# Kernel optimization log

Measured on AMD Instinct MI355X. Metric: run time of the kernel, lower is better.

The kernel has to match this reference:

```python
import jax, jax.numpy as jnp
import numpy as np

EPS = 1e-5

def conv1d(x, w, b, pad):
    # x: (B,Cin,T), w: (Cout,Cin,K)
    y = jax.lax.conv_general_dilated(x, w, (1,), [(pad, pad)],
                                     dimension_numbers=('NCW', 'OIW', 'NCW'))
    return y + b[None, :, None]

def group_norm(x, scale, bias, groups):
    B, C, T = x.shape
    xg = x.reshape(B, groups, C // groups, T)
    mu = xg.mean(axis=(2, 3), keepdims=True)
    var = xg.var(axis=(2, 3), keepdims=True)
    xn = ((xg - mu) * jax.lax.rsqrt(var + EPS)).reshape(B, C, T)
    return xn * scale[None, :, None] + bias[None, :, None]

def setup_inputs() -> dict:
    key = jax.random.key(0)
    ks = jax.random.split(key, 16)
    T, B = 1024, 128
    class_size, style_size, char_style_size = 80, 256, 64
    hidden, n_out = 128, 1
    cin = class_size + style_size + char_style_size  # 400
    def w(k, shape, fan_in):
        return jax.random.normal(k, shape, jnp.float32) * (1.0 / np.sqrt(fan_in))
    inp = {
        'input': jax.random.normal(ks[0], (T, B, class_size), jnp.float32),
        'g_style': jax.random.normal(ks[1], (B, style_size), jnp.float32),
        'spacing_style': jax.random.normal(ks[2], (B, 8), jnp.float32),
        'char_style': jax.random.normal(ks[3], (B, class_size, char_style_size), jnp.float32),
        'conv1_w': w(ks[4], (hidden, cin, 3), cin * 3),
        'conv1_b': jnp.zeros((hidden,), jnp.float32),
        'gn1_s': jnp.ones((hidden,), jnp.float32),
        'gn1_b': jnp.zeros((hidden,), jnp.float32),
        'conv2_w': w(ks[5], (hidden // 2, hidden, 3), hidden * 3),
        'conv2_b': jnp.zeros((hidden // 2,), jnp.float32),
        'gn2_s': jnp.ones((hidden // 2,), jnp.float32),
        'gn2_b': jnp.zeros((hidden // 2,), jnp.float32),
        'conv3_w': w(ks[6], (hidden // 4, hidden // 2, 3), (hidden // 2) * 3),
        'conv3_b': jnp.zeros((hidden // 4,), jnp.float32),
        'gn3_s': jnp.ones((hidden // 4,), jnp.float32),
        'gn3_b': jnp.zeros((hidden // 4,), jnp.float32),
        'conv4_w': w(ks[7], (n_out, hidden // 4, 1), hidden // 4),
        'conv4_b': jnp.zeros((n_out,), jnp.float32),
        'mean': jnp.full((1, n_out), 2.0, jnp.float32),
        'std': jnp.full((1, n_out), 1.0, jnp.float32),
    }
    return inp

def reference(input, g_style, spacing_style, char_style,
              conv1_w, conv1_b, gn1_s, gn1_b,
              conv2_w, conv2_b, gn2_s, gn2_b,
              conv3_w, conv3_b, gn3_s, gn3_b,
              conv4_w, conv4_b, mean, std):
    T, B, _ = input.shape
    # vectorized char-style gather (replaces the python double loop)
    text_chars = jnp.argmax(input, axis=2)                      # (T,B)
    input_style = char_style[jnp.arange(B)[None, :], text_chars]  # (T,B,Dc)
    gs = jnp.broadcast_to(g_style[None], (T,) + g_style.shape)    # (T,B,Ds)
    x = jnp.concatenate([input, gs, input_style], axis=2)         # (T,B,Cin)
    x = x.transpose(1, 2, 0)                                      # (B,Cin,T)
    x = jax.nn.relu(group_norm(conv1d(x, conv1_w, conv1_b, 1), gn1_s, gn1_b, 32))
    x = jax.nn.relu(group_norm(conv1d(x, conv2_w, conv2_b, 1), gn2_s, gn2_b, 32))
    x = jax.nn.relu(group_norm(conv1d(x, conv3_w, conv3_b, 1), gn3_s, gn3_b, 32))
    x = conv1d(x, conv4_w, conv4_b, 0)                            # (B,n_out,T)
    out = x.transpose(2, 0, 1)                                    # (T,B,n_out)
    return out * std + mean
```

## Files before the change

### kernel.cpp

```cpp
#include <hip/hip_runtime.h>
#include <hip/hip_bf16.h>

#define T_LEN 1024
#define BATCH 128
#define NM 131072

typedef __attribute__((ext_vector_type(8))) short short8;
typedef __attribute__((ext_vector_type(4))) float f32x4;

__device__ __forceinline__ float b2f(ushort u) {
  union { uint i; float f; } c; c.i = ((uint)u) << 16; return c.f;
}
__device__ __forceinline__ ushort f2b(float f) {
  __hip_bfloat16 h = __float2bfloat16(f);
  return *reinterpret_cast<ushort*>(&h);
}
__device__ __forceinline__ uint pack2(float a, float b) {
  return (uint)f2b(a) | ((uint)f2b(b) << 16);
}

__global__ __launch_bounds__(256) void k_prep(const float* __restrict__ inp, const float* __restrict__ cs,
    const float* __restrict__ gsty,
    const float* __restrict__ w1, const float* __restrict__ b1,
    const float* __restrict__ w2, const float* __restrict__ w3,
    ushort* __restrict__ X1, float* __restrict__ Gfull, float* __restrict__ Gk0, float* __restrict__ Gk2,
    ushort* __restrict__ Wp1, ushort* __restrict__ Wp2, ushort* __restrict__ Wp3) {
  int bid = blockIdx.x, tid = threadIdx.x;
  if (bid < 1024) {
    __shared__ __align__(16) ushort L[4][32][160];
    int b0 = (bid >> 5) * 4;
    int t0 = (bid & 31) * 32;
    int q = tid & 3;
    int u = tid >> 2;
    int bp = u & 3;
    int tpA = u >> 2;
    int tpB = tpA + 16;
    int mA = (t0 + tpA)*128 + b0 + bp;
    int mB = (t0 + tpB)*128 + b0 + bp;
    const float* rpA = inp + (size_t)mA*80 + q*20;
    const float* rpB = inp + (size_t)mB*80 + q*20;
    float va[20], vb[20];
    #pragma unroll
    for (int i = 0; i < 5; ++i) {
      float4 ua = *(const float4*)(rpA + i*4);
      va[i*4+0]=ua.x; va[i*4+1]=ua.y; va[i*4+2]=ua.z; va[i*4+3]=ua.w;
    }
    #pragma unroll
    for (int i = 0; i < 5; ++i) {
      float4 ub = *(const float4*)(rpB + i*4);
      vb[i*4+0]=ub.x; vb[i*4+1]=ub.y; vb[i*4+2]=ub.z; vb[i*4+3]=ub.w;
    }
    {
      float best = va[0]; int bi = q*20;
      #pragma unroll
      for (int i = 1; i < 20; ++i) if (va[i] > best) { best = va[i]; bi = q*20 + i; }
      #pragma unroll
      for (int d = 1; d <= 2; d <<= 1) {
        float ob = __shfl_xor(best, d);
        int   oi = __shfl_xor(bi, d);
        if (ob > best || (ob == best && oi < bi)) { best = ob; bi = oi; }
      }
      ushort* lr = &L[bp][tpA][0];
      #pragma unroll
      for (int i = 0; i < 5; ++i) {
        uint2 pk; pk.x = pack2(va[i*4], va[i*4+1]); pk.y = pack2(va[i*4+2], va[i*4+3]);
        *(uint2*)(lr + q*20 + i*4) = pk;
      }
      *(uint2*)(lr + 80 + q*4) = make_uint2(0u, 0u);
      const float* crow = cs + ((size_t)(b0+bp)*80 + bi)*64 + q*16;
      #pragma unroll
      for (int i = 0; i < 4; ++i) {
        float4 uu = *(const float4*)(crow + i*4);
        uint2 pk; pk.x = pack2(uu.x, uu.y); pk.y = pack2(uu.z, uu.w);
        *(uint2*)(lr + 96 + q*16 + i*4) = pk;
      }
    }
    {
      float best = vb[0]; int bi = q*20;
      #pragma unroll
      for (int i = 1; i < 20; ++i) if (vb[i] > best) { best = vb[i]; bi = q*20 + i; }
      #pragma unroll
      for (int d = 1; d <= 2; d <<= 1) {
        float ob = __shfl_xor(best, d);
        int   oi = __shfl_xor(bi, d);
        if (ob > best || (ob == best && oi < bi)) { best = ob; bi = oi; }
      }
      ushort* lr = &L[bp][tpB][0];
      #pragma unroll
      for (int i = 0; i < 5; ++i) {
        uint2 pk; pk.x = pack2(vb[i*4], vb[i*4+1]); pk.y = pack2(vb[i*4+2], vb[i*4+3]);
        *(uint2*)(lr + q*20 + i*4) = pk;
      }
      *(uint2*)(lr + 80 + q*4) = make_uint2(0u, 0u);
      const float* crow = cs + ((size_t)(b0+bp)*80 + bi)*64 + q*16;
      #pragma unroll
      for (int i = 0; i < 4; ++i) {
        float4 uu = *(const float4*)(crow + i*4);
        uint2 pk; pk.x = pack2(uu.x, uu.y); pk.y = pack2(uu.z, uu.w);
        *(uint2*)(lr + 96 + q*16 + i*4) = pk;
      }
    }
    __syncthreads();
    int wave = tid >> 6, lane = tid & 63;
    ushort* dst = X1 + ((size_t)(b0 + wave)*1024 + t0)*160;
    const ushort* src = &L[wave][0][0];
    #pragma unroll
    for (int it = 0; it < 10; ++it) {
      int r = it*64 + lane;
      *(uint4*)(dst + r*8) = *(const uint4*)(src + r*8);
    }
  } else if (bid < 1152) {
    int b = bid - 1024;
    __shared__ float gl[256];
    gl[tid] = gsty[b*256 + tid];
    __syncthreads();
    if (tid < 128) {
      int o = tid;
      const float* wr = w1 + (size_t)o*1200 + 240;
      float s0 = 0.f, s1 = 0.f, s2 = 0.f;
      for (int c = 0; c < 256; ++c) {
        float g = gl[c];
        s0 += wr[c*3+0]*g; s1 += wr[c*3+1]*g; s2 += wr[c*3+2]*g;
      }
      Gk0[b*128+o] = s0;
      Gk2[b*128+o] = s2;
      Gfull[b*128+o] = s0 + s1 + s2 + b1[o];
    }
  } else {
    int e = (bid - 1152)*256 + tid;
    if (e < 61440) {
      int o = e / 480, r = e % 480, k = r / 160, c = r % 160;
      float v = 0.f;
      if (c < 80)       v = w1[(size_t)o*1200 + c*3 + k];
      else if (c >= 96) v = w1[(size_t)o*1200 + (336 + (c-96))*3 + k];
      Wp1[e] = f2b(v);
    } else if (e < 61440 + 24576) {
      int e2 = e - 61440;
      int o = e2/384, r = e2%384, k = r/128, c = r%128;
      Wp2[e2] = f2b(w2[(size_t)o*384 + c*3 + k]);
    } else if (e < 61440 + 24576 + 6144) {
      int e3 = e - 61440 - 24576;
      int o = e3/192, r = e3%192, k = r/64, c = r%64;
      Wp3[e3] = f2b(w3[(size_t)o*192 + c*3 + k]);
    }
  }
}

__device__ __forceinline__ uint4 c1_ldx(const ushort* X1b, int cc, int t0, int task) {
  int r = task >> 2, q = task & 3;
  int t = t0 - 1 + r;
  if (t >= 0 && t < T_LEN) return *(const uint4*)(X1b + (size_t)t*160 + cc*32 + q*8);
  return make_uint4(0u,0u,0u,0u);
}
__device__ __forceinline__ short8 c1_ldw(const ushort* Wp1, int cc, int task) {
  int o = task / 12, seg = task % 12;
  int k = seg >> 2, oct = seg & 3;
  return *(const short8*)(Wp1 + (size_t)o*480 + k*160 + cc*32 + oct*8);
}
__device__ __forceinline__ void c1_wrx(ushort (*Xsb)[40], int task, uint4 v) {
  int r = task >> 2, q = task & 3;
  *(uint4*)&Xsb[r][q*8] = v;
}
__device__ __forceinline__ void c1_wrw(ushort (*Wsb)[104], int task, short8 v) {
  int o = task / 12, seg = task % 12;
  *(short8*)&Wsb[o][seg*8] = v;
}

__global__ __launch_bounds__(256) void k_conv1(const ushort* __restrict__ X1, const ushort* __restrict__ Wp1,
    const float* __restrict__ Gfull, const float* __restrict__ Gk0, const float* __restrict__ Gk2,
    ushort* __restrict__ y1, float2* __restrict__ part1) {
  __shared__ __align__(16) ushort Xs[2][130][40];
  __shared__ __align__(16) ushort Ws[2][128][104];
  __shared__ float gf[128], g0v[128], g2v[128];
  __shared__ float ps[4][128], pq[4][128];
  int b = blockIdx.x, tt = blockIdx.y;
  int t0 = tt * 128;
  int tid = threadIdx.x, lane = tid & 63, wave = tid >> 6;
  int ln = lane & 15, lq = lane >> 4, wt = wave * 32;
  const ushort* X1b = X1 + (size_t)b * 163840;

  if (tid < 128) {
    gf[tid]  = Gfull[b*128 + tid];
    g0v[tid] = Gk0[b*128 + tid];
    g2v[tid] = Gk2[b*128 + tid];
  }
  f32x4 acc[2][8];
  #pragma unroll
  for (int m = 0; m < 2; ++m)
    #pragma unroll
    for (int n = 0; n < 8; ++n) { f32x4 z = {0.f,0.f,0.f,0.f}; acc[m][n] = z; }

  uint4 rx0, rx1, rx2;
  short8 rw[6];

  rx0 = c1_ldx(X1b, 0, t0, tid);
  rx1 = c1_ldx(X1b, 0, t0, tid + 256);
  if (tid < 8) rx2 = c1_ldx(X1b, 0, t0, tid + 512);
  #pragma unroll
  for (int i = 0; i < 6; ++i) rw[i] = c1_ldw(Wp1, 0, tid + i*256);
  c1_wrx(Xs[0], tid, rx0);
  c1_wrx(Xs[0], tid + 256, rx1);
  if (tid < 8) c1_wrx(Xs[0], tid + 512, rx2);
  #pragma unroll
  for (int i = 0; i < 6; ++i) c1_wrw(Ws[0], tid + i*256, rw[i]);
  __syncthreads();

  for (int cc = 0; cc < 5; ++cc) {
    bool more = (cc < 4);
    if (more) {
      rx0 = c1_ldx(X1b, cc+1, t0, tid);
      rx1 = c1_ldx(X1b, cc+1, t0, tid + 256);
      if (tid < 8) rx2 = c1_ldx(X1b, cc+1, t0, tid + 512);
      #pragma unroll
      for (int i = 0; i < 6; ++i) rw[i] = c1_ldw(Wp1, cc+1, tid + i*256);
    }
    int cur = cc & 1;
    #pragma unroll
    for (int k = 0; k < 3; ++k) {
      short8 a0 = *(const short8*)&Xs[cur][wt + ln + k][lq*8];
      short8 a1 = *(const short8*)&Xs[cur][wt + 16 + ln + k][lq*8];
      #pragma unroll
      for (int nt = 0; nt < 8; ++nt) {
        short8 bb = *(const short8*)&Ws[cur][nt*16 + ln][k*32 + lq*8];
        acc[0][nt] = __builtin_amdgcn_mfma_f32_16x16x32_bf16(a0, bb, acc[0][nt], 0, 0, 0);
        acc[1][nt] = __builtin_amdgcn_mfma_f32_16x16x32_bf16(a1, bb, acc[1][nt], 0, 0, 0);
      }
    }
    if (more) {
      int nxt = cur ^ 1;
      c1_wrx(Xs[nxt], tid, rx0);
      c1_wrx(Xs[nxt], tid + 256, rx1);
      if (tid < 8) c1_wrx(Xs[nxt], tid + 512, rx2);
      #pragma unroll
      for (int i = 0; i < 6; ++i) c1_wrw(Ws[nxt], tid + i*256, rw[i]);
    }
    __syncthreads();
  }

  #pragma unroll
  for (int nt = 0; nt < 8; ++nt) {
    int o = nt*16 + ln;
    float add = gf[o];
    float s = 0.f, sq = 0.f;
    #pragma unroll
    for (int mt = 0; mt < 2; ++mt) {
      int tb = t0 + wt + mt*16 + lq*4;
      float vv[4];
      #pragma unroll
      for (int r = 0; r < 4; ++r) {
        float v = acc[mt][nt][r] + add;
        int t = tb + r;
        if (t == 0) v -= g0v[o];
        if (t == T_LEN-1) v -= g2v[o];
        vv[r] = v; s += v; sq += v*v;
      }
      uint2 pk;
      pk.x = pack2(vv[0], vv[1]);
      pk.y = pack2(vv[2], vv[3]);
      *(uint2*)(y1 + ((size_t)b*128 + o)*T_LEN + tb) = pk;
    }
    s  += __shfl_xor(s, 16);  s  += __shfl_xor(s, 32);
    sq += __shfl_xor(sq, 16); sq += __shfl_xor(sq, 32);
    if (lane < 16) { ps[wave][o] = s; pq[wave][o] = sq; }
  }
  __syncthreads();
  if (tid < 128) {
    float S = ps[0][tid]+ps[1][tid]+ps[2][tid]+ps[3][tid];
    float Q = pq[0][tid]+pq[1][tid]+pq[2][tid]+pq[3][tid];
    part1[((size_t)b*128 + tid)*8 + tt] = make_float2(S, Q);
  }
}

__device__ __forceinline__ short8 mid_ldw(const ushort* Wp, int cin, int cc, int task) {
  int o = task / 12, seg = task % 12;
  int k = seg >> 2, oct = seg & 3;
  return *(const short8*)(Wp + ((size_t)o*3 + k)*cin + cc*32 + oct*8);
}
__device__ __forceinline__ void mid_wrw(ushort (*Wsb)[104], int task, short8 v) {
  int o = task / 12, seg = task % 12;
  *(short8*)&Wsb[o][seg*8] = v;
}

template<int NC, int CO, int NT, int CPG>
__global__ __launch_bounds__(256) void k_convmid(const ushort* __restrict__ xin,
    const ushort* __restrict__ Wp, const float* __restrict__ bias,
    const float2* __restrict__ partin, const float* __restrict__ gs, const float* __restrict__ gb,
    ushort* __restrict__ yout, float2* __restrict__ part) {
  constexpr int CIN = NC*32;
  constexpr int NG = CIN/CPG;
  __shared__ __align__(16) ushort Xs[2][130][40];
  __shared__ __align__(16) ushort Ws[2][CO][104];
  __shared__ float2 affl[CIN];
  __shared__ float ssb[CIN], qqb[CIN];
  __shared__ float2 gmr[NG];
  __shared__ float bl[CO];
  __shared__ float ps[4][CO], pq[4][CO];
  int b = blockIdx.x, tt = blockIdx.y, t0 = tt*128;
  int tid = threadIdx.x, lane = tid & 63, wave = tid >> 6;
  int ln = lane & 15, lq = lane >> 4, wt = wave*32;
  int cp = (tid & 15)*2, j = tid >> 4;
  int er = (tid < 32) ? 0 : 129, eci = tid & 31;
  const ushort* xb = xin + (size_t)b * CIN * T_LEN;

  if (tid < CIN) {
    const float2* p = partin + (size_t)(b*CIN + tid)*8;
    float S = 0.f, Q = 0.f;
    #pragma unroll
    for (int j2 = 0; j2 < 8; ++j2) { float2 v = p[j2]; S += v.x; Q += v.y; }
    ssb[tid] = S; qqb[tid] = Q;
  }
  if (tid < CO)  bl[tid]  = bias[tid];

  f32x4 acc[2][NT];
  #pragma unroll
  for (int m = 0; m < 2; ++m)
    #pragma unroll
    for (int n = 0; n < NT; ++n) { f32x4 z = {0.f,0.f,0.f,0.f}; acc[m][n] = z; }

  short8 v0, v1;
  ushort ev = 0;
  short8 rw0, rw1, rw2;
  int te = t0 - 1 + er;

  {
    const ushort* s0 = xb + (size_t)cp * T_LEN + t0 + j*8;
    v0 = *(const short8*)s0;
    v1 = *(const short8*)(s0 + T_LEN);
    ev = 0;
    if (tid < 64 && te >= 0 && te < T_LEN) ev = xb[(size_t)eci * T_LEN + te];
    rw0 = mid_ldw(Wp, CIN, 0, tid);
    if constexpr (CO == 64) {
      rw1 = mid_ldw(Wp, CIN, 0, tid + 256);
      rw2 = mid_ldw(Wp, CIN, 0, tid + 512);
    } else {
      if (tid < 128) rw1 = mid_ldw(Wp, CIN, 0, tid + 256);
    }
  }
  __syncthreads();
  if (tid < NG) {
    float S = 0.f, Q = 0.f;
    #pragma unroll
    for (int ci = 0; ci < CPG; ++ci) { S += ssb[tid*CPG+ci]; Q += qqb[tid*CPG+ci]; }
    float invn = 1.f / (float)(CPG * T_LEN);
    float m = S * invn;
    float var = Q * invn - m*m;
    gmr[tid] = make_float2(m, rsqrtf(var + 1e-5f));
  }
  __syncthreads();
  if (tid < CIN) {
    float2 mr = gmr[tid / CPG];
    float a = mr.y * gs[tid];
    affl[tid] = make_float2(a, gb[tid] - mr.x * a);
  }
  __syncthreads();
  {
    float2 A0 = affl[cp], A1 = affl[cp+1];
    #pragma unroll
    for (int e = 0; e < 8; ++e) {
      float f0 = fmaxf(0.f, b2f((ushort)v0[e])*A0.x + A0.y);
      float f1 = fmaxf(0.f, b2f((ushort)v1[e])*A1.x + A1.y);
      *(uint*)&Xs[0][1 + j*8 + e][cp] = pack2(f0, f1);
    }
    if (tid < 64) {
      ushort val = 0;
      if (te >= 0 && te < T_LEN) { float2 A = affl[eci]; val = f2b(fmaxf(0.f, b2f(ev)*A.x + A.y)); }
      Xs[0][er][eci] = val;
    }
    mid_wrw(Ws[0], tid, rw0);
    if constexpr (CO == 64) {
      mid_wrw(Ws[0], tid + 256, rw1);
      mid_wrw(Ws[0], tid + 512, rw2);
    } else {
      if (tid < 128) mid_wrw(Ws[0], tid + 256, rw1);
    }
  }
  __syncthreads();

  for (int cc = 0; cc < NC; ++cc) {
    bool more = (cc + 1 < NC);
    if (more) {
      const ushort* s0 = xb + (size_t)((cc+1)*32 + cp) * T_LEN + t0 + j*8;
      v0 = *(const short8*)s0;
      v1 = *(const short8*)(s0 + T_LEN);
      ev = 0;
      if (tid < 64 && te >= 0 && te < T_LEN) ev = xb[(size_t)((cc+1)*32 + eci) * T_LEN + te];
      rw0 = mid_ldw(Wp, CIN, cc+1, tid);
      if constexpr (CO == 64) {
        rw1 = mid_ldw(Wp, CIN, cc+1, tid + 256);
        rw2 = mid_ldw(Wp, CIN, cc+1, tid + 512);
      } else {
        if (tid < 128) rw1 = mid_ldw(Wp, CIN, cc+1, tid + 256);
      }
    }
    int cur = cc & 1;
    #pragma unroll
    for (int k = 0; k < 3; ++k) {
      short8 a0 = *(const short8*)&Xs[cur][wt + ln + k][lq*8];
      short8 a1 = *(const short8*)&Xs[cur][wt + 16 + ln + k][lq*8];
      #pragma unroll
      for (int nt = 0; nt < NT; ++nt) {
        short8 bb = *(const short8*)&Ws[cur][nt*16 + ln][k*32 + lq*8];
        acc[0][nt] = __builtin_amdgcn_mfma_f32_16x16x32_bf16(a0, bb, acc[0][nt], 0, 0, 0);
        acc[1][nt] = __builtin_amdgcn_mfma_f32_16x16x32_bf16(a1, bb, acc[1][nt], 0, 0, 0);
      }
    }
    if (more) {
      int nxt = cur ^ 1;
      float2 A0 = affl[(cc+1)*32 + cp], A1 = affl[(cc+1)*32 + cp + 1];
      #pragma unroll
      for (int e = 0; e < 8; ++e) {
        float f0 = fmaxf(0.f, b2f((ushort)v0[e])*A0.x + A0.y);
        float f1 = fmaxf(0.f, b2f((ushort)v1[e])*A1.x + A1.y);
        *(uint*)&Xs[nxt][1 + j*8 + e][cp] = pack2(f0, f1);
      }
      if (tid < 64) {
        ushort val = 0;
        if (te >= 0 && te < T_LEN) { float2 A = affl[(cc+1)*32 + eci]; val = f2b(fmaxf(0.f, b2f(ev)*A.x + A.y)); }
        Xs[nxt][er][eci] = val;
      }
      mid_wrw(Ws[nxt], tid, rw0);
      if constexpr (CO == 64) {
        mid_wrw(Ws[nxt], tid + 256, rw1);
        mid_wrw(Ws[nxt], tid + 512, rw2);
      } else {
        if (tid < 128) mid_wrw(Ws[nxt], tid + 256, rw1);
      }
    }
    __syncthreads();
  }

  #pragma unroll
  for (int nt = 0; nt < NT; ++nt) {
    int o = nt*16 + ln;
    float add = bl[o];
    float s = 0.f, sq = 0.f;
    #pragma unroll
    for (int mt = 0; mt < 2; ++mt) {
      int tb = t0 + wt + mt*16 + lq*4;
      float vv[4];
      #pragma unroll
      for (int r = 0; r < 4; ++r) {
        float v = acc[mt][nt][r] + add;
        vv[r] = v; s += v; sq += v*v;
      }
      uint2 pk;
      pk.x = pack2(vv[0], vv[1]);
      pk.y = pack2(vv[2], vv[3]);
      *(uint2*)(yout + ((size_t)b*CO + o)*T_LEN + tb) = pk;
    }
    s  += __shfl_xor(s, 16);  s  += __shfl_xor(s, 32);
    sq += __shfl_xor(sq, 16); sq += __shfl_xor(sq, 32);
    if (lane < 16) { ps[wave][o] = s; pq[wave][o] = sq; }
  }
  __syncthreads();
  if (tid < CO) {
    float S = ps[0][tid]+ps[1][tid]+ps[2][tid]+ps[3][tid];
    float Q = pq[0][tid]+pq[1][tid]+pq[2][tid]+pq[3][tid];
    part[((size_t)b*CO + tid)*8 + tt] = make_float2(S, Q);
  }
}

__global__ __launch_bounds__(256) void k_final(const ushort* __restrict__ y3, const float2* __restrict__ part3,
    const float* __restrict__ s3, const float* __restrict__ b3,
    const float* __restrict__ w4, const float* __restrict__ b4,
    const float* __restrict__ mn, const float* __restrict__ sd, float* __restrict__ out) {
  int b = blockIdx.x;
  int t = blockIdx.y * 256 + threadIdx.x;
  __shared__ float wl[32];
  __shared__ float2 al[32];
  if (threadIdx.x < 32) {
    int c = threadIdx.x;
    const float2* p = part3 + (size_t)(b*32 + c)*8;
    float S = 0.f, Q = 0.f;
    #pragma unroll
    for (int j = 0; j < 8; ++j) { float2 v = p[j]; S += v.x; Q += v.y; }
    float invn = 1.f / (float)T_LEN;
    float m = S * invn;
    float var = Q * invn - m*m;
    float rs = rsqrtf(var + 1e-5f);
    float a = rs * s3[c];
    al[c] = make_float2(a, b3[c] - m*a);
    wl[c] = w4[c];
  }
  __syncthreads();
  float s = b4[0];
  #pragma unroll 8
  for (int c = 0; c < 32; ++c) {
    float v = b2f(y3[((size_t)b*32 + c)*T_LEN + t]);
    float2 A = al[c];
    s += wl[c] * fmaxf(0.f, v*A.x + A.y);
  }
  out[(size_t)t*BATCH + b] = s*sd[0] + mn[0];
}

extern "C" void kernel_launch(void* const* d_in, const int* in_sizes, int n_in,
                              void* d_out, int out_size, void* d_ws, size_t ws_size,
                              hipStream_t stream) {
  const float* inp  = (const float*)d_in[0];
  const float* gsty = (const float*)d_in[1];
  const float* cs   = (const float*)d_in[3];
  const float* w1   = (const float*)d_in[4];
  const float* b1   = (const float*)d_in[5];
  const float* gn1s = (const float*)d_in[6];
  const float* gn1b = (const float*)d_in[7];
  const float* w2   = (const float*)d_in[8];
  const float* b2   = (const float*)d_in[9];
  const float* gn2s = (const float*)d_in[10];
  const float* gn2b = (const float*)d_in[11];
  const float* w3   = (const float*)d_in[12];
  const float* b3   = (const float*)d_in[13];
  const float* gn3s = (const float*)d_in[14];
  const float* gn3b = (const float*)d_in[15];
  const float* w4   = (const float*)d_in[16];
  const float* b4   = (const float*)d_in[17];
  const float* mn   = (const float*)d_in[18];
  const float* sd   = (const float*)d_in[19];
  float* out = (float*)d_out;
  ushort* wsu = (ushort*)d_ws;

  ushort* X1  = wsu;
  ushort* Wp1 = X1 + (size_t)20971520;
  ushort* Wp2 = Wp1 + 61440;
  ushort* Wp3 = Wp2 + 24576;
  float* Gfull = (float*)(Wp3 + 6144);
  float* Gk0   = Gfull + 16384;
  float* Gk2   = Gk0 + 16384;
  ushort* y1 = (ushort*)(Gk2 + 16384);
  ushort* y2 = y1 + (size_t)NM*128;
  ushort* y3 = y2 + (size_t)NM*64;
  float2* part1 = (float2*)(y3 + (size_t)NM*32);
  float2* part2 = part1 + 131072;
  float2* part3 = part2 + 65536;

  k_prep<<<1512, 256, 0, stream>>>(inp, cs, gsty, w1, b1, w2, w3,
                                   X1, Gfull, Gk0, Gk2, Wp1, Wp2, Wp3);
  k_conv1<<<dim3(128,8), 256, 0, stream>>>(X1, Wp1, Gfull, Gk0, Gk2, y1, part1);
  k_convmid<4,64,4,4><<<dim3(128,8), 256, 0, stream>>>(y1, Wp2, b2, part1, gn1s, gn1b, y2, part2);
  k_convmid<2,32,2,2><<<dim3(128,8), 256, 0, stream>>>(y2, Wp3, b3, part2, gn2s, gn2b, y3, part3);
  k_final<<<dim3(128,4), 256, 0, stream>>>(y3, part3, gn3s, gn3b, w4, b4, mn, sd, out);
}
```

Measured before the change: 95.95 us.

## Read one-hot input directly in conv1 and shrink intermediate buffer to char-style only

The prep kernel no longer writes the 80 input channels plus padding into a 160-wide bf16 staging tensor. It now stores only the 64 gathered char-style channels. conv1 reads and converts the fp32 input channels straight from the original tensor for the first three channel chunks, and reads the compact char-style buffer for the last two. This cuts the staging buffer's write and read traffic. In exchange, conv1 loads fp32 data with strided per-timestep access (stride B*80) and does the bf16 conversion itself.

New measurement: 95.56 us. About the same (-0.4%).

```diff
diff --git a/kernel.cpp b/kernel.cpp
--- a/kernel.cpp
+++ b/kernel.cpp
@@ -23,18 +23,17 @@
     const float* __restrict__ gsty,
     const float* __restrict__ w1, const float* __restrict__ b1,
     const float* __restrict__ w2, const float* __restrict__ w3,
-    ushort* __restrict__ X1, float* __restrict__ Gfull, float* __restrict__ Gk0, float* __restrict__ Gk2,
+    ushort* __restrict__ X1c, float* __restrict__ Gfull, float* __restrict__ Gk0, float* __restrict__ Gk2,
     ushort* __restrict__ Wp1, ushort* __restrict__ Wp2, ushort* __restrict__ Wp3) {
   int bid = blockIdx.x, tid = threadIdx.x;
   if (bid < 1024) {
-    __shared__ __align__(16) ushort L[4][32][160];
+    __shared__ __align__(16) ushort Lc[4][32][64];
     int b0 = (bid >> 5) * 4;
     int t0 = (bid & 31) * 32;
     int q = tid & 3;
     int u = tid >> 2;
     int bp = u & 3;
-    int tpA = u >> 2;
-    int tpB = tpA + 16;
+    int tpA = u >> 2, tpB = tpA + 16;
     int mA = (t0 + tpA)*128 + b0 + bp;
     int mB = (t0 + tpB)*128 + b0 + bp;
     const float* rpA = inp + (size_t)mA*80 + q*20;
@@ -60,19 +59,13 @@
         int   oi = __shfl_xor(bi, d);
         if (ob > best || (ob == best && oi < bi)) { best = ob; bi = oi; }
       }
-      ushort* lr = &L[bp][tpA][0];
-      #pragma unroll
-      for (int i = 0; i < 5; ++i) {
-        uint2 pk; pk.x = pack2(va[i*4], va[i*4+1]); pk.y = pack2(va[i*4+2], va[i*4+3]);
-        *(uint2*)(lr + q*20 + i*4) = pk;
-      }
-      *(uint2*)(lr + 80 + q*4) = make_uint2(0u, 0u);
+      ushort* lr = &Lc[bp][tpA][0];
       const float* crow = cs + ((size_t)(b0+bp)*80 + bi)*64 + q*16;
       #pragma unroll
       for (int i = 0; i < 4; ++i) {
         float4 uu = *(const float4*)(crow + i*4);
         uint2 pk; pk.x = pack2(uu.x, uu.y); pk.y = pack2(uu.z, uu.w);
-        *(uint2*)(lr + 96 + q*16 + i*4) = pk;
+        *(uint2*)(lr + q*16 + i*4) = pk;
       }
     }
     {
@@ -85,27 +78,21 @@
         int   oi = __shfl_xor(bi, d);
         if (ob > best || (ob == best && oi < bi)) { best = ob; bi = oi; }
       }
-      ushort* lr = &L[bp][tpB][0];
-      #pragma unroll
-      for (int i = 0; i < 5; ++i) {
-        uint2 pk; pk.x = pack2(vb[i*4], vb[i*4+1]); pk.y = pack2(vb[i*4+2], vb[i*4+3]);
-        *(uint2*)(lr + q*20 + i*4) = pk;
-      }
-      *(uint2*)(lr + 80 + q*4) = make_uint2(0u, 0u);
+      ushort* lr = &Lc[bp][tpB][0];
       const float* crow = cs + ((size_t)(b0+bp)*80 + bi)*64 + q*16;
       #pragma unroll
       for (int i = 0; i < 4; ++i) {
         float4 uu = *(const float4*)(crow + i*4);
         uint2 pk; pk.x = pack2(uu.x, uu.y); pk.y = pack2(uu.z, uu.w);
-        *(uint2*)(lr + 96 + q*16 + i*4) = pk;
+        *(uint2*)(lr + q*16 + i*4) = pk;
       }
     }
     __syncthreads();
     int wave = tid >> 6, lane = tid & 63;
-    ushort* dst = X1 + ((size_t)(b0 + wave)*1024 + t0)*160;
-    const ushort* src = &L[wave][0][0];
-    #pragma unroll
-    for (int it = 0; it < 10; ++it) {
+    ushort* dst = X1c + ((size_t)(b0 + wave)*1024 + t0)*64;
+    const ushort* src = &Lc[wave][0][0];
+    #pragma unroll
+    for (int it = 0; it < 4; ++it) {
       int r = it*64 + lane;
       *(uint4*)(dst + r*8) = *(const uint4*)(src + r*8);
     }
@@ -146,11 +133,29 @@
   }
 }
 
-__device__ __forceinline__ uint4 c1_ldx(const ushort* X1b, int cc, int t0, int task) {
+__device__ __forceinline__ void c1_ldf(const float* __restrict__ inp, int b, int cc, int t0, int task,
+                                       float4& fa, float4& fb) {
   int r = task >> 2, q = task & 3;
   int t = t0 - 1 + r;
-  if (t >= 0 && t < T_LEN) return *(const uint4*)(X1b + (size_t)t*160 + cc*32 + q*8);
+  int c8 = cc*32 + q*8;
+  fa = make_float4(0.f,0.f,0.f,0.f); fb = fa;
+  if (t >= 0 && t < T_LEN && c8 < 80) {
+    const float* src = inp + ((size_t)t*BATCH + b)*80 + c8;
+    fa = *(const float4*)src;
+    fb = *(const float4*)(src + 4);
+  }
+}
+__device__ __forceinline__ uint4 c1_ldc(const ushort* X1cb, int cc, int t0, int task) {
+  int r = task >> 2, q = task & 3;
+  int t = t0 - 1 + r;
+  if (t >= 0 && t < T_LEN) return *(const uint4*)(X1cb + (size_t)t*64 + (cc-3)*32 + q*8);
   return make_uint4(0u,0u,0u,0u);
+}
+__device__ __forceinline__ uint4 packf(float4 a, float4 b) {
+  uint4 p;
+  p.x = pack2(a.x, a.y); p.y = pack2(a.z, a.w);
+  p.z = pack2(b.x, b.y); p.w = pack2(b.z, b.w);
+  return p;
 }
 __device__ __forceinline__ short8 c1_ldw(const ushort* Wp1, int cc, int task) {
   int o = task / 12, seg = task % 12;
@@ -166,7 +171,8 @@
   *(short8*)&Wsb[o][seg*8] = v;
 }
 
-__global__ __launch_bounds__(256) void k_conv1(const ushort* __restrict__ X1, const ushort* __restrict__ Wp1,
+__global__ __launch_bounds__(256) void k_conv1(const float* __restrict__ inp, const ushort* __restrict__ X1c,
+    const ushort* __restrict__ Wp1,
     const float* __restrict__ Gfull, const float* __restrict__ Gk0, const float* __restrict__ Gk2,
     ushort* __restrict__ y1, float2* __restrict__ part1) {
   __shared__ __align__(16) ushort Xs[2][130][40];
@@ -177,7 +183,7 @@
   int t0 = tt * 128;
   int tid = threadIdx.x, lane = tid & 63, wave = tid >> 6;
   int ln = lane & 15, lq = lane >> 4, wt = wave * 32;
-  const ushort* X1b = X1 + (size_t)b * 163840;
+  const ushort* X1cb = X1c + (size_t)b * 65536;
 
   if (tid < 128) {
     gf[tid]  = Gfull[b*128 + tid];
@@ -190,27 +196,35 @@
     #pragma unroll
     for (int n = 0; n < 8; ++n) { f32x4 z = {0.f,0.f,0.f,0.f}; acc[m][n] = z; }
 
+  float4 fa0, fb0, fa1, fb1, fa2, fb2;
   uint4 rx0, rx1, rx2;
   short8 rw[6];
 
-  rx0 = c1_ldx(X1b, 0, t0, tid);
-  rx1 = c1_ldx(X1b, 0, t0, tid + 256);
-  if (tid < 8) rx2 = c1_ldx(X1b, 0, t0, tid + 512);
+  c1_ldf(inp, b, 0, t0, tid, fa0, fb0);
+  c1_ldf(inp, b, 0, t0, tid + 256, fa1, fb1);
+  if (tid < 8) c1_ldf(inp, b, 0, t0, tid + 512, fa2, fb2);
   #pragma unroll
   for (int i = 0; i < 6; ++i) rw[i] = c1_ldw(Wp1, 0, tid + i*256);
-  c1_wrx(Xs[0], tid, rx0);
-  c1_wrx(Xs[0], tid + 256, rx1);
-  if (tid < 8) c1_wrx(Xs[0], tid + 512, rx2);
+  c1_wrx(Xs[0], tid, packf(fa0, fb0));
+  c1_wrx(Xs[0], tid + 256, packf(fa1, fb1));
+  if (tid < 8) c1_wrx(Xs[0], tid + 512, packf(fa2, fb2));
   #pragma unroll
   for (int i = 0; i < 6; ++i) c1_wrw(Ws[0], tid + i*256, rw[i]);
   __syncthreads();
 
   for (int cc = 0; cc < 5; ++cc) {
     bool more = (cc < 4);
+    bool nf = (cc + 1 < 3);
     if (more) {
-      rx0 = c1_ldx(X1b, cc+1, t0, tid);
-      rx1 = c1_ldx(X1b, cc+1, t0, tid + 256);
-      if (tid < 8) rx2 = c1_ldx(X1b, cc+1, t0, tid + 512);
+      if (nf) {
+        c1_ldf(inp, b, cc+1, t0, tid, fa0, fb0);
+        c1_ldf(inp, b, cc+1, t0, tid + 256, fa1, fb1);
+        if (tid < 8) c1_ldf(inp, b, cc+1, t0, tid + 512, fa2, fb2);
+      } else {
+        rx0 = c1_ldc(X1cb, cc+1, t0, tid);
+        rx1 = c1_ldc(X1cb, cc+1, t0, tid + 256);
+        if (tid < 8) rx2 = c1_ldc(X1cb, cc+1, t0, tid + 512);
+      }
       #pragma unroll
       for (int i = 0; i < 6; ++i) rw[i] = c1_ldw(Wp1, cc+1, tid + i*256);
     }
@@ -228,9 +242,15 @@
     }
     if (more) {
       int nxt = cur ^ 1;
-      c1_wrx(Xs[nxt], tid, rx0);
-      c1_wrx(Xs[nxt], tid + 256, rx1);
-      if (tid < 8) c1_wrx(Xs[nxt], tid + 512, rx2);
+      if (nf) {
+        c1_wrx(Xs[nxt], tid, packf(fa0, fb0));
+        c1_wrx(Xs[nxt], tid + 256, packf(fa1, fb1));
+        if (tid < 8) c1_wrx(Xs[nxt], tid + 512, packf(fa2, fb2));
+      } else {
+        c1_wrx(Xs[nxt], tid, rx0);
+        c1_wrx(Xs[nxt], tid + 256, rx1);
+        if (tid < 8) c1_wrx(Xs[nxt], tid + 512, rx2);
+      }
       #pragma unroll
       for (int i = 0; i < 6; ++i) c1_wrw(Ws[nxt], tid + i*256, rw[i]);
     }
@@ -518,8 +538,8 @@
   float* out = (float*)d_out;
   ushort* wsu = (ushort*)d_ws;
 
-  ushort* X1  = wsu;
-  ushort* Wp1 = X1 + (size_t)20971520;
+  ushort* X1c = wsu;
+  ushort* Wp1 = X1c + (size_t)8388608;
   ushort* Wp2 = Wp1 + 61440;
   ushort* Wp3 = Wp2 + 24576;
   float* Gfull = (float*)(Wp3 + 6144);
@@ -533,8 +553,8 @@
   float2* part3 = part2 + 65536;
 
   k_prep<<<1512, 256, 0, stream>>>(inp, cs, gsty, w1, b1, w2, w3,
-                                   X1, Gfull, Gk0, Gk2, Wp1, Wp2, Wp3);
-  k_conv1<<<dim3(128,8), 256, 0, stream>>>(X1, Wp1, Gfull, Gk0, Gk2, y1, part1);
+                                   X1c, Gfull, Gk0, Gk2, Wp1, Wp2, Wp3);
+  k_conv1<<<dim3(128,8), 256, 0, stream>>>(inp, X1c, Wp1, Gfull, Gk0, Gk2, y1, part1);
   k_convmid<4,64,4,4><<<dim3(128,8), 256, 0, stream>>>(y1, Wp2, b2, part1, gn1s, gn1b, y2, part2);
   k_convmid<2,32,2,2><<<dim3(128,8), 256, 0, stream>>>(y2, Wp3, b3, part2, gn2s, gn2b, y3, part3);
   k_final<<<dim3(128,4), 256, 0, stream>>>(y3, part3, gn3s, gn3b, w4, b4, mn, sd, out);
```
